# Performance work log

Measured on AMD Instinct MI355X. Metric: run time of the kernel, lower is better.

Reference implementation:

```python
import jax, jax.numpy as jnp
import numpy as np

B, S, H, C = 256, 256, 768, 150  # batch, seq_len, hidden_size, total class prototypes


def setup_inputs() -> dict:
    key = jax.random.key(0)
    k1, k2, k3 = jax.random.split(key, 3)
    last_hidden_state = jax.random.normal(k1, (B, S, H), dtype=jnp.float32)
    attention_mask = jnp.ones((B, S), dtype=jnp.int32)
    means = jax.random.normal(k2, (C, H), dtype=jnp.float32)
    A = jax.random.normal(k3, (H, H), dtype=jnp.float32) / np.sqrt(H)
    # symmetric PSD-ish inverse-covariance, like pinv of a covariance (hermitian)
    cov_inv = A @ A.T + jnp.eye(H, dtype=jnp.float32)
    return {"last_hidden_state": last_hidden_state, "attention_mask": attention_mask,
            "means": means, "cov_inv": cov_inv}


def reference(last_hidden_state, attention_mask, means, cov_inv):
    # mean pooling over valid tokens: [B, S, H] -> [B, H]
    m = attention_mask[..., None].astype(last_hidden_state.dtype)
    prelogits = (last_hidden_state * m).sum(axis=1) / jnp.clip(m.sum(axis=1), 1e-9, None)
    # mahalanobis score per class, vectorized over all C prototypes:
    xS = prelogits @ cov_inv                      # [B, H]
    t_x = jnp.sum(xS * prelogits, axis=-1)        # [B]
    mS = means @ cov_inv                          # [C, H]
    t_m = jnp.sum(mS * means, axis=-1)            # [C]
    scores = t_x[:, None] - 2.0 * (xS @ means.T) + t_m[None, :]  # [B, C]
    scores_over_tasks = scores.T                  # [C, B], matches torch.stack/cat layout
    indices = jnp.argmin(scores_over_tasks, axis=0)  # [B]
    return indices, scores_over_tasks
```

## Files before the change

kernel.cpp:

```cpp
#include <hip/hip_runtime.h>
#include <hip/hip_bf16.h>

#define B 256
#define S 256
#define H 768
#define C 150
#define H4 192


__global__ __launch_bounds__(192) void kPool(const float* __restrict__ lhs,
                                             const int* __restrict__ mask,
                                             float* __restrict__ part1,
                                             int* __restrict__ cntp) {
    const int bid = blockIdx.x;
    const int t = threadIdx.x;
    __shared__ float msk[64];

    const int b = bid >> 2, chunk = bid & 3, s0 = chunk * 64;
    if (t < 64) {
        const int mv = mask[b * S + s0 + t];
        msk[t] = (float)mv;
        int v = mv;
#pragma unroll
        for (int off = 32; off > 0; off >>= 1) v += __shfl_down(v, off, 64);
        if (t == 0) cntp[b * 4 + chunk] = v;
    }
    __syncthreads();

    const float4* src = (const float4*)lhs + (size_t)(b * S + s0) * H4 + t;
    float4 acc = make_float4(0.f, 0.f, 0.f, 0.f);
#pragma unroll 8
    for (int s = 0; s < 64; ++s) {
        const float m = msk[s];
        const float4 v = src[(size_t)s * H4];
        acc.x += v.x * m; acc.y += v.y * m; acc.z += v.z * m; acc.w += v.w * m;
    }
    ((float4*)part1)[(size_t)(b * 4 + chunk) * H4 + t] = acc;
}

__global__ __launch_bounds__(192) void kC(const float* __restrict__ part1,
                                          const int* __restrict__ cntp,
                                          const float* __restrict__ cov,
                                          const float* __restrict__ means,
                                          float* __restrict__ dp,
                                          float* __restrict__ tx_part,
                                          float* __restrict__ tm_part) {
    const int t = threadIdx.x;
    const int kg = t / 24, c4 = t % 24;
    __shared__ float xsl[8 * H];
    __shared__ float4 red2[8][24];
    __shared__ float4 xsf[8][24];
    __shared__ float sred[8][3];

    if (blockIdx.x < 256) {
        const int rt = blockIdx.x >> 3, cs = blockIdx.x & 7;
        const int r0 = rt * 8, cb = cs * 24;

        for (int r = 0; r < 8; ++r) {
            const int row = r0 + r;
            const int cnt = cntp[row * 4] + cntp[row * 4 + 1] + cntp[row * 4 + 2] + cntp[row * 4 + 3];
            const float inv = 1.0f / fmaxf((float)cnt, 1e-9f);
            const float4* p = (const float4*)part1 + (size_t)row * 4 * H4 + t;
            const float4 a = p[0], b2 = p[H4], c2 = p[2 * H4], d2 = p[3 * H4];
            float4 v;
            v.x = (a.x + b2.x + c2.x + d2.x) * inv;
            v.y = (a.y + b2.y + c2.y + d2.y) * inv;
            v.z = (a.z + b2.z + c2.z + d2.z) * inv;
            v.w = (a.w + b2.w + c2.w + d2.w) * inv;
            ((float4*)xsl)[r * H4 + t] = v;
        }
        __syncthreads();

        float4 acc[8];
#pragma unroll
        for (int r = 0; r < 8; ++r) acc[r] = make_float4(0.f, 0.f, 0.f, 0.f);
        const float4* cov4 = (const float4*)cov + cb + c4;
#pragma unroll 4
        for (int kk = 0; kk < 96; ++kk) {
            const int k = kg * 96 + kk;
            const float4 cv = cov4[(size_t)k * H4];
#pragma unroll
            for (int r = 0; r < 8; ++r) {
                const float xv = xsl[r * H + k];
                acc[r].x += xv * cv.x; acc[r].y += xv * cv.y;
                acc[r].z += xv * cv.z; acc[r].w += xv * cv.w;
            }
        }

        float pdr[8];
#pragma unroll
        for (int r = 0; r < 8; ++r) pdr[r] = 0.f;
        for (int r = 0; r < 8; ++r) {
            red2[kg][c4] = acc[r];
            __syncthreads();
            if (kg == 0) {
                float4 s = red2[0][c4];
#pragma unroll
                for (int g = 1; g < 8; ++g) {
                    const float4 q = red2[g][c4];
                    s.x += q.x; s.y += q.y; s.z += q.z; s.w += q.w;
                }
                xsf[r][c4] = s;
                const float4 xv = ((float4*)xsl)[r * H4 + cb + c4];
                pdr[r] = s.x * xv.x + s.y * xv.y + s.z * xv.z + s.w * xv.w;
            }
            __syncthreads();
        }

        if (t < 64) {
#pragma unroll
            for (int r = 0; r < 8; ++r) {
                float v = (t < 24) ? pdr[r] : 0.f;
#pragma unroll
                for (int off = 16; off > 0; off >>= 1) v += __shfl_down(v, off, 32);
                if (t == 0) tx_part[cs * 256 + r0 + r] = v;
            }
        }

        if (t < C) {
            const float4* mu4 = (const float4*)means + (size_t)t * H4 + cb;
            float a8[8];
#pragma unroll
            for (int r = 0; r < 8; ++r) a8[r] = 0.f;
#pragma unroll 4
            for (int j = 0; j < 24; ++j) {
                const float4 mv = mu4[j];
#pragma unroll
                for (int r = 0; r < 8; ++r) {
                    const float4 x = xsf[r][j];
                    a8[r] += mv.x * x.x + mv.y * x.y + mv.z * x.z + mv.w * x.w;
                }
            }
#pragma unroll
            for (int r = 0; r < 8; ++r)
                dp[((size_t)(cs * 256) + (r0 + r)) * 150 + t] = a8[r];
        }
    } else {
        const int idx = blockIdx.x - 256;
        const int rt = idx >> 3, cs = idx & 7;
        const int r0 = rt * 8, cb = cs * 24;

        for (int r = 0; r < 8; ++r) {
            const int row = r0 + r;
            float4 v = make_float4(0.f, 0.f, 0.f, 0.f);
            if (row < C) v = ((const float4*)means)[(size_t)row * H4 + t];
            ((float4*)xsl)[r * H4 + t] = v;
        }
        __syncthreads();

        float4 acc[8];
#pragma unroll
        for (int r = 0; r < 8; ++r) acc[r] = make_float4(0.f, 0.f, 0.f, 0.f);
        const float4* cov4 = (const float4*)cov + cb + c4;
#pragma unroll 4
        for (int kk = 0; kk < 96; ++kk) {
            const int k = kg * 96 + kk;
            const float4 cv = cov4[(size_t)k * H4];
#pragma unroll
            for (int r = 0; r < 8; ++r) {
                const float xv = xsl[r * H + k];
                acc[r].x += xv * cv.x; acc[r].y += xv * cv.y;
                acc[r].z += xv * cv.z; acc[r].w += xv * cv.w;
            }
        }
        const int w = t >> 6;
#pragma unroll
        for (int r = 0; r < 8; ++r) {
            const float4 mu = ((float4*)xsl)[r * H4 + cb + c4];
            float pd = acc[r].x * mu.x + acc[r].y * mu.y + acc[r].z * mu.z + acc[r].w * mu.w;
#pragma unroll
            for (int off = 32; off > 0; off >>= 1) pd += __shfl_down(pd, off, 64);
            if ((t & 63) == 0) sred[r][w] = pd;
        }
        __syncthreads();
        if (t < 8) {
            const int row = r0 + t;
            if (row < C)
                tm_part[cs * 152 + row] = sred[t][0] + sred[t][1] + sred[t][2];
        }
    }
}

__global__ __launch_bounds__(192) void kD(const float* __restrict__ dp,
                                          const float* __restrict__ tx_part,
                                          const float* __restrict__ tm_part,
                                          float* __restrict__ out) {
    const int b = blockIdx.x, t = threadIdx.x;
    __shared__ float sv[192];
    __shared__ int si[192];

    float sc = INFINITY;
    if (t < C) {
        float d = 0.f;
#pragma unroll
        for (int j = 0; j < 8; ++j) d += dp[((size_t)(j * 256) + b) * 150 + t];
        float tx = 0.f;
#pragma unroll
        for (int j = 0; j < 8; ++j) tx += tx_part[j * 256 + b];
        float tm = 0.f;
#pragma unroll
        for (int j = 0; j < 8; ++j) tm += tm_part[j * 152 + t];
        sc = tx - 2.0f * d + tm;
        out[B + (size_t)t * B + b] = sc;
    }
    sv[t] = sc;
    si[t] = (t < C) ? t : 0x7fffffff;
    __syncthreads();
#pragma unroll
    for (int off = 96; off >= 3; off >>= 1) {
        if (t < off) {
            const float ov = sv[t + off];
            const int oi = si[t + off];
            if (ov < sv[t] || (ov == sv[t] && oi < si[t])) { sv[t] = ov; si[t] = oi; }
        }
        __syncthreads();
    }
    if (t == 0) {
        float bv = sv[0];
        int bi = si[0];
#pragma unroll
        for (int j = 1; j < 3; ++j)
            if (sv[j] < bv || (sv[j] == bv && si[j] < bi)) { bv = sv[j]; bi = si[j]; }
        out[b] = (float)bi;
    }
}

extern "C" void kernel_launch(void* const* d_in, const int* in_sizes, int n_in,
                              void* d_out, int out_size, void* d_ws, size_t ws_size,
                              hipStream_t stream) {
    const float* lhs   = (const float*)d_in[0];
    const int*   mask  = (const int*)d_in[1];
    const float* means = (const float*)d_in[2];
    const float* cov   = (const float*)d_in[3];
    float* out = (float*)d_out;

    char* ws = (char*)d_ws;
    float* part1   = (float*)(ws + 0);
    float* dp      = (float*)(ws + 3145728);
    float* tx_part = (float*)(ws + 4374528);
    float* tm_part = (float*)(ws + 4382720);
    int*   cntp    = (int*)  (ws + 4387584);

    kPool<<<dim3(1024), 192, 0, stream>>>(lhs, mask, part1, cntp);
    kC<<<dim3(256 + 152), 192, 0, stream>>>(part1, cntp, cov, means, dp, tx_part, tm_part);
    kD<<<dim3(256), 192, 0, stream>>>(dp, tx_part, tm_part, out);
}
```

Before: 59.22 us.

## Fuse means·cov term into pooling launch and finalize scores via last-block ticket

The t_m computation (means @ cov · means) moves into the pooling kernel as extra blocks, restructured to 4 rows × 96-k slices. The final score and argmin kernel is folded into the main GEMM kernel: the last of the 8 column-slice blocks per row tile, chosen with an atomic ticket, does the reduction and argmin for its 8 rows. This drops one kernel launch and shortens the dependency chain, and the pooling blocks can overlap with the t_m work. It adds a memset, a threadfence and serialized finalization in 32 winner blocks.

```diff
diff --git a/kernel.cpp b/kernel.cpp
--- a/kernel.cpp
+++ b/kernel.cpp
@@ -8,220 +8,234 @@
 #define H4 192
 
 
-__global__ __launch_bounds__(192) void kPool(const float* __restrict__ lhs,
-                                             const int* __restrict__ mask,
-                                             float* __restrict__ part1,
-                                             int* __restrict__ cntp) {
+__global__ __launch_bounds__(192) void kPoolTm(const float* __restrict__ lhs,
+                                               const int* __restrict__ mask,
+                                               const float* __restrict__ means,
+                                               const float* __restrict__ cov,
+                                               float* __restrict__ part1,
+                                               int* __restrict__ cntp,
+                                               float* __restrict__ tm_part) {
     const int bid = blockIdx.x;
     const int t = threadIdx.x;
-    __shared__ float msk[64];
-
-    const int b = bid >> 2, chunk = bid & 3, s0 = chunk * 64;
-    if (t < 64) {
-        const int mv = mask[b * S + s0 + t];
-        msk[t] = (float)mv;
-        int v = mv;
-#pragma unroll
-        for (int off = 32; off > 0; off >>= 1) v += __shfl_down(v, off, 64);
-        if (t == 0) cntp[b * 4 + chunk] = v;
-    }
-    __syncthreads();
-
-    const float4* src = (const float4*)lhs + (size_t)(b * S + s0) * H4 + t;
-    float4 acc = make_float4(0.f, 0.f, 0.f, 0.f);
+    __shared__ float shbuf[4 * H];
+    __shared__ float red[4][3];
+
+    if (bid < 1024) {
+        const int b = bid >> 2, chunk = bid & 3, s0 = chunk * 64;
+        float* msk = shbuf;
+        if (t < 64) {
+            const int mv = mask[b * S + s0 + t];
+            msk[t] = (float)mv;
+            int v = mv;
+#pragma unroll
+            for (int off = 32; off > 0; off >>= 1) v += __shfl_down(v, off, 64);
+            if (t == 0) cntp[b * 4 + chunk] = v;
+        }
+        __syncthreads();
+
+        const float4* src = (const float4*)lhs + (size_t)(b * S + s0) * H4 + t;
+        float4 acc = make_float4(0.f, 0.f, 0.f, 0.f);
 #pragma unroll 8
-    for (int s = 0; s < 64; ++s) {
-        const float m = msk[s];
-        const float4 v = src[(size_t)s * H4];
-        acc.x += v.x * m; acc.y += v.y * m; acc.z += v.z * m; acc.w += v.w * m;
-    }
-    ((float4*)part1)[(size_t)(b * 4 + chunk) * H4 + t] = acc;
+        for (int s = 0; s < 64; ++s) {
+            const float m = msk[s];
+            const float4 v = src[(size_t)s * H4];
+            acc.x += v.x * m; acc.y += v.y * m; acc.z += v.z * m; acc.w += v.w * m;
+        }
+        ((float4*)part1)[(size_t)(b * 4 + chunk) * H4 + t] = acc;
+    } else {
+        const int idx = bid - 1024;
+        const int rg = idx >> 3, ks = idx & 7;
+        const int r0 = rg * 4, k0 = ks * 96;
+
+#pragma unroll
+        for (int r = 0; r < 4; ++r) {
+            const int row = r0 + r;
+            float4 v = make_float4(0.f, 0.f, 0.f, 0.f);
+            if (row < C) v = ((const float4*)means)[(size_t)row * H4 + t];
+            ((float4*)shbuf)[r * H4 + t] = v;
+        }
+        __syncthreads();
+
+        float4 acc[4];
+#pragma unroll
+        for (int r = 0; r < 4; ++r) acc[r] = make_float4(0.f, 0.f, 0.f, 0.f);
+        const float4* cov4 = (const float4*)cov + t;
+#pragma unroll 4
+        for (int kk = 0; kk < 96; ++kk) {
+            const int k = k0 + kk;
+            const float4 cv = cov4[(size_t)k * H4];
+#pragma unroll
+            for (int r = 0; r < 4; ++r) {
+                const float xv = shbuf[r * H + k];
+                acc[r].x += xv * cv.x; acc[r].y += xv * cv.y;
+                acc[r].z += xv * cv.z; acc[r].w += xv * cv.w;
+            }
+        }
+        const int w = t >> 6;
+#pragma unroll
+        for (int r = 0; r < 4; ++r) {
+            const float4 mu = ((float4*)shbuf)[r * H4 + t];
+            float pd = acc[r].x * mu.x + acc[r].y * mu.y + acc[r].z * mu.z + acc[r].w * mu.w;
+#pragma unroll
+            for (int off = 32; off > 0; off >>= 1) pd += __shfl_down(pd, off, 64);
+            if ((t & 63) == 0) red[r][w] = pd;
+        }
+        __syncthreads();
+        if (t < 4) {
+            const int row = r0 + t;
+            if (row < C)
+                tm_part[ks * 152 + row] = red[t][0] + red[t][1] + red[t][2];
+        }
+    }
 }
 
-__global__ __launch_bounds__(192) void kC(const float* __restrict__ part1,
-                                          const int* __restrict__ cntp,
-                                          const float* __restrict__ cov,
-                                          const float* __restrict__ means,
-                                          float* __restrict__ dp,
-                                          float* __restrict__ tx_part,
-                                          float* __restrict__ tm_part) {
+__global__ __launch_bounds__(192) void kCF(const float* __restrict__ part1,
+                                           const int* __restrict__ cntp,
+                                           const float* __restrict__ cov,
+                                           const float* __restrict__ means,
+                                           float* __restrict__ dp,
+                                           float* __restrict__ tx_part,
+                                           const float* __restrict__ tm_part,
+                                           int* __restrict__ ticket,
+                                           float* __restrict__ out) {
+    const int rt = blockIdx.x >> 3, cs = blockIdx.x & 7;
+    const int r0 = rt * 8, cb = cs * 24;
     const int t = threadIdx.x;
     const int kg = t / 24, c4 = t % 24;
     __shared__ float xsl[8 * H];
     __shared__ float4 red2[8][24];
     __shared__ float4 xsf[8][24];
-    __shared__ float sred[8][3];
-
-    if (blockIdx.x < 256) {
-        const int rt = blockIdx.x >> 3, cs = blockIdx.x & 7;
-        const int r0 = rt * 8, cb = cs * 24;
-
-        for (int r = 0; r < 8; ++r) {
-            const int row = r0 + r;
-            const int cnt = cntp[row * 4] + cntp[row * 4 + 1] + cntp[row * 4 + 2] + cntp[row * 4 + 3];
-            const float inv = 1.0f / fmaxf((float)cnt, 1e-9f);
-            const float4* p = (const float4*)part1 + (size_t)row * 4 * H4 + t;
-            const float4 a = p[0], b2 = p[H4], c2 = p[2 * H4], d2 = p[3 * H4];
-            float4 v;
-            v.x = (a.x + b2.x + c2.x + d2.x) * inv;
-            v.y = (a.y + b2.y + c2.y + d2.y) * inv;
-            v.z = (a.z + b2.z + c2.z + d2.z) * inv;
-            v.w = (a.w + b2.w + c2.w + d2.w) * inv;
-            ((float4*)xsl)[r * H4 + t] = v;
-        }
-        __syncthreads();
-
-        float4 acc[8];
-#pragma unroll
-        for (int r = 0; r < 8; ++r) acc[r] = make_float4(0.f, 0.f, 0.f, 0.f);
-        const float4* cov4 = (const float4*)cov + cb + c4;
-#pragma unroll 4
-        for (int kk = 0; kk < 96; ++kk) {
-            const int k = kg * 96 + kk;
-            const float4 cv = cov4[(size_t)k * H4];
-#pragma unroll
-            for (int r = 0; r < 8; ++r) {
-                const float xv = xsl[r * H + k];
-                acc[r].x += xv * cv.x; acc[r].y += xv * cv.y;
-                acc[r].z += xv * cv.z; acc[r].w += xv * cv.w;
-            }
-        }
-
-        float pdr[8];
-#pragma unroll
-        for (int r = 0; r < 8; ++r) pdr[r] = 0.f;
-        for (int r = 0; r < 8; ++r) {
-            red2[kg][c4] = acc[r];
-            __syncthreads();
-            if (kg == 0) {
-                float4 s = red2[0][c4];
-#pragma unroll
-                for (int g = 1; g < 8; ++g) {
-                    const float4 q = red2[g][c4];
-                    s.x += q.x; s.y += q.y; s.z += q.z; s.w += q.w;
-                }
-                xsf[r][c4] = s;
-                const float4 xv = ((float4*)xsl)[r * H4 + cb + c4];
-                pdr[r] = s.x * xv.x + s.y * xv.y + s.z * xv.z + s.w * xv.w;
-            }
-            __syncthreads();
-        }
-
-        if (t < 64) {
-#pragma unroll
-            for (int r = 0; r < 8; ++r) {
-                float v = (t < 24) ? pdr[r] : 0.f;
-#pragma unroll
-                for (int off = 16; off > 0; off >>= 1) v += __shfl_down(v, off, 32);
-                if (t == 0) tx_part[cs * 256 + r0 + r] = v;
-            }
-        }
-
-        if (t < C) {
-            const float4* mu4 = (const float4*)means + (size_t)t * H4 + cb;
-            float a8[8];
-#pragma unroll
-            for (int r = 0; r < 8; ++r) a8[r] = 0.f;
-#pragma unroll 4
-            for (int j = 0; j < 24; ++j) {
-                const float4 mv = mu4[j];
-#pragma unroll
-                for (int r = 0; r < 8; ++r) {
-                    const float4 x = xsf[r][j];
-                    a8[r] += mv.x * x.x + mv.y * x.y + mv.z * x.z + mv.w * x.w;
-                }
-            }
-#pragma unroll
-            for (int r = 0; r < 8; ++r)
-                dp[((size_t)(cs * 256) + (r0 + r)) * 150 + t] = a8[r];
-        }
-    } else {
-        const int idx = blockIdx.x - 256;
-        const int rt = idx >> 3, cs = idx & 7;
-        const int r0 = rt * 8, cb = cs * 24;
-
-        for (int r = 0; r < 8; ++r) {
-            const int row = r0 + r;
-            float4 v = make_float4(0.f, 0.f, 0.f, 0.f);
-            if (row < C) v = ((const float4*)means)[(size_t)row * H4 + t];
-            ((float4*)xsl)[r * H4 + t] = v;
-        }
-        __syncthreads();
-
-        float4 acc[8];
-#pragma unroll
-        for (int r = 0; r < 8; ++r) acc[r] = make_float4(0.f, 0.f, 0.f, 0.f);
-        const float4* cov4 = (const float4*)cov + cb + c4;
-#pragma unroll 4
-        for (int kk = 0; kk < 96; ++kk) {
-            const int k = kg * 96 + kk;
-            const float4 cv = cov4[(size_t)k * H4];
-#pragma unroll
-            for (int r = 0; r < 8; ++r) {
-                const float xv = xsl[r * H + k];
-                acc[r].x += xv * cv.x; acc[r].y += xv * cv.y;
-                acc[r].z += xv * cv.z; acc[r].w += xv * cv.w;
-            }
-        }
-        const int w = t >> 6;
-#pragma unroll
-        for (int r = 0; r < 8; ++r) {
-            const float4 mu = ((float4*)xsl)[r * H4 + cb + c4];
-            float pd = acc[r].x * mu.x + acc[r].y * mu.y + acc[r].z * mu.z + acc[r].w * mu.w;
-#pragma unroll
-            for (int off = 32; off > 0; off >>= 1) pd += __shfl_down(pd, off, 64);
-            if ((t & 63) == 0) sred[r][w] = pd;
-        }
-        __syncthreads();
-        if (t < 8) {
-            const int row = r0 + t;
-            if (row < C)
-                tm_part[cs * 152 + row] = sred[t][0] + sred[t][1] + sred[t][2];
-        }
-    }
-}
-
-__global__ __launch_bounds__(192) void kD(const float* __restrict__ dp,
-                                          const float* __restrict__ tx_part,
-                                          const float* __restrict__ tm_part,
-                                          float* __restrict__ out) {
-    const int b = blockIdx.x, t = threadIdx.x;
     __shared__ float sv[192];
     __shared__ int si[192];
-
-    float sc = INFINITY;
+    __shared__ int winflag;
+
+    for (int r = 0; r < 8; ++r) {
+        const int row = r0 + r;
+        const int cnt = cntp[row * 4] + cntp[row * 4 + 1] + cntp[row * 4 + 2] + cntp[row * 4 + 3];
+        const float inv = 1.0f / fmaxf((float)cnt, 1e-9f);
+        const float4* p = (const float4*)part1 + (size_t)row * 4 * H4 + t;
+        const float4 a = p[0], b2 = p[H4], c2 = p[2 * H4], d2 = p[3 * H4];
+        float4 v;
+        v.x = (a.x + b2.x + c2.x + d2.x) * inv;
+        v.y = (a.y + b2.y + c2.y + d2.y) * inv;
+        v.z = (a.z + b2.z + c2.z + d2.z) * inv;
+        v.w = (a.w + b2.w + c2.w + d2.w) * inv;
+        ((float4*)xsl)[r * H4 + t] = v;
+    }
+    __syncthreads();
+
+    float4 acc[8];
+#pragma unroll
+    for (int r = 0; r < 8; ++r) acc[r] = make_float4(0.f, 0.f, 0.f, 0.f);
+    const float4* cov4 = (const float4*)cov + cb + c4;
+#pragma unroll 4
+    for (int kk = 0; kk < 96; ++kk) {
+        const int k = kg * 96 + kk;
+        const float4 cv = cov4[(size_t)k * H4];
+#pragma unroll
+        for (int r = 0; r < 8; ++r) {
+            const float xv = xsl[r * H + k];
+            acc[r].x += xv * cv.x; acc[r].y += xv * cv.y;
+            acc[r].z += xv * cv.z; acc[r].w += xv * cv.w;
+        }
+    }
+
+    float pdr[8];
+#pragma unroll
+    for (int r = 0; r < 8; ++r) pdr[r] = 0.f;
+    for (int r = 0; r < 8; ++r) {
+        red2[kg][c4] = acc[r];
+        __syncthreads();
+        if (kg == 0) {
+            float4 s = red2[0][c4];
+#pragma unroll
+            for (int g = 1; g < 8; ++g) {
+                const float4 q = red2[g][c4];
+                s.x += q.x; s.y += q.y; s.z += q.z; s.w += q.w;
+            }
+            xsf[r][c4] = s;
+            const float4 xv = ((float4*)xsl)[r * H4 + cb + c4];
+            pdr[r] = s.x * xv.x + s.y * xv.y + s.z * xv.z + s.w * xv.w;
+        }
+        __syncthreads();
+    }
+
+    if (t < 64) {
+#pragma unroll
+        for (int r = 0; r < 8; ++r) {
+            float v = (t < 24) ? pdr[r] : 0.f;
+#pragma unroll
+            for (int off = 16; off > 0; off >>= 1) v += __shfl_down(v, off, 32);
+            if (t == 0) tx_part[cs * 256 + r0 + r] = v;
+        }
+    }
+
     if (t < C) {
-        float d = 0.f;
-#pragma unroll
-        for (int j = 0; j < 8; ++j) d += dp[((size_t)(j * 256) + b) * 150 + t];
-        float tx = 0.f;
-#pragma unroll
-        for (int j = 0; j < 8; ++j) tx += tx_part[j * 256 + b];
-        float tm = 0.f;
-#pragma unroll
-        for (int j = 0; j < 8; ++j) tm += tm_part[j * 152 + t];
-        sc = tx - 2.0f * d + tm;
-        out[B + (size_t)t * B + b] = sc;
-    }
-    sv[t] = sc;
-    si[t] = (t < C) ? t : 0x7fffffff;
+        const float4* mu4 = (const float4*)means + (size_t)t * H4 + cb;
+        float a8[8];
+#pragma unroll
+        for (int r = 0; r < 8; ++r) a8[r] = 0.f;
+#pragma unroll 4
+        for (int j = 0; j < 24; ++j) {
+            const float4 mv = mu4[j];
+#pragma unroll
+            for (int r = 0; r < 8; ++r) {
+                const float4 x = xsf[r][j];
+                a8[r] += mv.x * x.x + mv.y * x.y + mv.z * x.z + mv.w * x.w;
+            }
+        }
+#pragma unroll
+        for (int r = 0; r < 8; ++r)
+            dp[((size_t)(cs * 256) + (r0 + r)) * 150 + t] = a8[r];
+    }
+
     __syncthreads();
-#pragma unroll
-    for (int off = 96; off >= 3; off >>= 1) {
-        if (t < off) {
-            const float ov = sv[t + off];
-            const int oi = si[t + off];
-            if (ov < sv[t] || (ov == sv[t] && oi < si[t])) { sv[t] = ov; si[t] = oi; }
-        }
-        __syncthreads();
-    }
     if (t == 0) {
-        float bv = sv[0];
-        int bi = si[0];
-#pragma unroll
-        for (int j = 1; j < 3; ++j)
-            if (sv[j] < bv || (sv[j] == bv && si[j] < bi)) { bv = sv[j]; bi = si[j]; }
-        out[b] = (float)bi;
+        __threadfence();
+        const int old = __hip_atomic_fetch_add(&ticket[rt], 1, __ATOMIC_ACQ_REL,
+                                               __HIP_MEMORY_SCOPE_AGENT);
+        winflag = (old == 7);
+    }
+    __syncthreads();
+    if (!winflag) return;
+
+    for (int r = 0; r < 8; ++r) {
+        const int row = r0 + r;
+        float sc = INFINITY;
+        if (t < C) {
+            float d = 0.f;
+#pragma unroll
+            for (int j = 0; j < 8; ++j) d += dp[((size_t)(j * 256) + row) * 150 + t];
+            float tx = 0.f;
+#pragma unroll
+            for (int j = 0; j < 8; ++j) tx += tx_part[j * 256 + row];
+            float tm = 0.f;
+#pragma unroll
+            for (int j = 0; j < 8; ++j) tm += tm_part[j * 152 + t];
+            sc = tx - 2.0f * d + tm;
+            out[B + (size_t)t * B + row] = sc;
+        }
+        sv[t] = sc;
+        si[t] = (t < C) ? t : 0x7fffffff;
+        __syncthreads();
+#pragma unroll
+        for (int off = 96; off >= 3; off >>= 1) {
+            if (t < off) {
+                const float ov = sv[t + off];
+                const int oi = si[t + off];
+                if (ov < sv[t] || (ov == sv[t] && oi < si[t])) { sv[t] = ov; si[t] = oi; }
+            }
+            __syncthreads();
+        }
+        if (t == 0) {
+            float bv = sv[0];
+            int bi = si[0];
+#pragma unroll
+            for (int j = 1; j < 3; ++j)
+                if (sv[j] < bv || (sv[j] == bv && si[j] < bi)) { bv = sv[j]; bi = si[j]; }
+            out[row] = (float)bi;
+        }
+        __syncthreads();
     }
 }
 
@@ -233,15 +247,16 @@
     const float* means = (const float*)d_in[2];
     const float* cov   = (const float*)d_in[3];
     float* out = (float*)d_out;
-
     char* ws = (char*)d_ws;
+
     float* part1   = (float*)(ws + 0);
     float* dp      = (float*)(ws + 3145728);
     float* tx_part = (float*)(ws + 4374528);
     float* tm_part = (float*)(ws + 4382720);
     int*   cntp    = (int*)  (ws + 4387584);
-
-    kPool<<<dim3(1024), 192, 0, stream>>>(lhs, mask, part1, cntp);
-    kC<<<dim3(256 + 152), 192, 0, stream>>>(part1, cntp, cov, means, dp, tx_part, tm_part);
-    kD<<<dim3(256), 192, 0, stream>>>(dp, tx_part, tm_part, out);
+    int*   ticket  = (int*)  (ws + 4391680);
+
+    hipMemsetAsync(ticket, 0, 128, stream);
+    kPoolTm<<<dim3(1024 + 304), 192, 0, stream>>>(lhs, mask, means, cov, part1, cntp, tm_part);
+    kCF<<<dim3(256), 192, 0, stream>>>(part1, cntp, cov, means, dp, tx_part, tm_part, ticket, out);
 }
```

Result: slower. 87.82 us (+48.3%).

## Finalize mean pooling inside kPool with one block per batch row

Applied to the files above, without the earlier changes.

The pooling kernel now runs one 384-thread block per batch row. Two halves of the sequence are reduced in registers and combined through shared memory, and the masked count is computed in the same block, so kPool writes the final normalized prelogits directly. This removes the 4-way partial-sum buffer and the extra reduction and count work that kC did for every column-split block, shrinking the workspace traffic. The trade-off is fewer blocks (256 instead of 1024) with longer serial loops, which may reduce the memory-level parallelism available for streaming the 200MB input.

```diff
diff --git a/kernel.cpp b/kernel.cpp
--- a/kernel.cpp
+++ b/kernel.cpp
@@ -8,38 +8,51 @@
 #define H4 192
 
 
-__global__ __launch_bounds__(192) void kPool(const float* __restrict__ lhs,
+__global__ __launch_bounds__(384) void kPool(const float* __restrict__ lhs,
                                              const int* __restrict__ mask,
-                                             float* __restrict__ part1,
-                                             int* __restrict__ cntp) {
-    const int bid = blockIdx.x;
+                                             float* __restrict__ prelogits) {
+    const int b = blockIdx.x;
     const int t = threadIdx.x;
-    __shared__ float msk[64];
-
-    const int b = bid >> 2, chunk = bid & 3, s0 = chunk * 64;
-    if (t < 64) {
-        const int mv = mask[b * S + s0 + t];
-        msk[t] = (float)mv;
-        int v = mv;
+    const int h = t / H4, c4 = t - h * H4;
+    __shared__ float msk[S];
+    __shared__ float4 hbuf[H4];
+    __shared__ float cntsh;
+
+    if (t < S) msk[t] = (float)mask[b * S + t];
+    __syncthreads();
+
+    if (t >= 320) {
+        const int idx = t - 320;
+        float v = msk[idx] + msk[idx + 64] + msk[idx + 128] + msk[idx + 192];
 #pragma unroll
         for (int off = 32; off > 0; off >>= 1) v += __shfl_down(v, off, 64);
-        if (t == 0) cntp[b * 4 + chunk] = v;
-    }
-    __syncthreads();
-
-    const float4* src = (const float4*)lhs + (size_t)(b * S + s0) * H4 + t;
+        if (idx == 0) cntsh = v;
+    }
+
+    const float4* src = (const float4*)lhs + (size_t)(b * S + h * 128) * H4 + c4;
+    const float* mrow = msk + h * 128;
     float4 acc = make_float4(0.f, 0.f, 0.f, 0.f);
 #pragma unroll 8
-    for (int s = 0; s < 64; ++s) {
-        const float m = msk[s];
+    for (int s = 0; s < 128; ++s) {
+        const float m = mrow[s];
         const float4 v = src[(size_t)s * H4];
         acc.x += v.x * m; acc.y += v.y * m; acc.z += v.z * m; acc.w += v.w * m;
     }
-    ((float4*)part1)[(size_t)(b * 4 + chunk) * H4 + t] = acc;
-}
-
-__global__ __launch_bounds__(192) void kC(const float* __restrict__ part1,
-                                          const int* __restrict__ cntp,
+    if (h == 1) hbuf[c4] = acc;
+    __syncthreads();
+    if (h == 0) {
+        const float4 o = hbuf[c4];
+        const float inv = 1.0f / fmaxf(cntsh, 1e-9f);
+        float4 r;
+        r.x = (acc.x + o.x) * inv;
+        r.y = (acc.y + o.y) * inv;
+        r.z = (acc.z + o.z) * inv;
+        r.w = (acc.w + o.w) * inv;
+        ((float4*)prelogits)[(size_t)b * H4 + c4] = r;
+    }
+}
+
+__global__ __launch_bounds__(192) void kC(const float* __restrict__ prelogits,
                                           const float* __restrict__ cov,
                                           const float* __restrict__ means,
                                           float* __restrict__ dp,
@@ -56,19 +69,9 @@
         const int rt = blockIdx.x >> 3, cs = blockIdx.x & 7;
         const int r0 = rt * 8, cb = cs * 24;
 
-        for (int r = 0; r < 8; ++r) {
-            const int row = r0 + r;
-            const int cnt = cntp[row * 4] + cntp[row * 4 + 1] + cntp[row * 4 + 2] + cntp[row * 4 + 3];
-            const float inv = 1.0f / fmaxf((float)cnt, 1e-9f);
-            const float4* p = (const float4*)part1 + (size_t)row * 4 * H4 + t;
-            const float4 a = p[0], b2 = p[H4], c2 = p[2 * H4], d2 = p[3 * H4];
-            float4 v;
-            v.x = (a.x + b2.x + c2.x + d2.x) * inv;
-            v.y = (a.y + b2.y + c2.y + d2.y) * inv;
-            v.z = (a.z + b2.z + c2.z + d2.z) * inv;
-            v.w = (a.w + b2.w + c2.w + d2.w) * inv;
-            ((float4*)xsl)[r * H4 + t] = v;
-        }
+#pragma unroll
+        for (int r = 0; r < 8; ++r)
+            ((float4*)xsl)[r * H4 + t] = ((const float4*)prelogits)[(size_t)(r0 + r) * H4 + t];
         __syncthreads();
 
         float4 acc[8];
@@ -233,15 +236,14 @@
     const float* means = (const float*)d_in[2];
     const float* cov   = (const float*)d_in[3];
     float* out = (float*)d_out;
-
     char* ws = (char*)d_ws;
-    float* part1   = (float*)(ws + 0);
-    float* dp      = (float*)(ws + 3145728);
-    float* tx_part = (float*)(ws + 4374528);
-    float* tm_part = (float*)(ws + 4382720);
-    int*   cntp    = (int*)  (ws + 4387584);
-
-    kPool<<<dim3(1024), 192, 0, stream>>>(lhs, mask, part1, cntp);
-    kC<<<dim3(256 + 152), 192, 0, stream>>>(part1, cntp, cov, means, dp, tx_part, tm_part);
+
+    float* prelogits = (float*)(ws + 0);
+    float* dp        = (float*)(ws + 786432);
+    float* tx_part   = (float*)(ws + 2015232);
+    float* tm_part   = (float*)(ws + 2023424);
+
+    kPool<<<dim3(B), 384, 0, stream>>>(lhs, mask, prelogits);
+    kC<<<dim3(256 + 152), 192, 0, stream>>>(prelogits, cov, means, dp, tx_part, tm_part);
     kD<<<dim3(256), 192, 0, stream>>>(dp, tx_part, tm_part, out);
 }
```

Measured after the change: 56.52 us. -4.6%, faster.
